# Optimization experiments

Hardware: AMD Instinct MI355X
Metric: run time of the kernel (lower is better)

## Reference

```python
import jax, jax.numpy as jnp
import numpy as np

B, P, N = 32, 64, 8192
EPS_CASE = 0.0001  # hard-coded threshold in fc_of_edge's tf.where


def setup_inputs() -> dict:
    key = jax.random.key(0)
    k1, k2 = jax.random.split(key)
    points = jax.random.normal(k1, (B, P, 2), dtype=jnp.float32)
    # phi grid comes from fc_tensor[0, 0, :] in the original ctor; use angles in [0, 2*pi)
    phi = jax.random.uniform(k2, (N,), dtype=jnp.float32) * (2.0 * np.pi)
    return {"points": points, "phi": phi}


def reference(points, phi):
    # q(phi) = [cos(phi), sin(phi) - 1], shape [2, N]
    q = jnp.stack([jnp.cos(phi), jnp.sin(phi) - 1.0])
    cross = jnp.array([[0.0, -1.0], [1.0, 0.0]], dtype=points.dtype)
    q_cross = cross @ q                                   # [2, N]
    scale = 1.0 / jnp.abs(q[0] ** 2 + q[1] ** 2)          # [N], real

    # vectorize the python edge loop: edge k is (points[:, k-1], points[:, k])
    p1 = points                                           # [B, P, 2]
    p0 = jnp.roll(points, 1, axis=1)                      # [B, P, 2]
    d = p1 - p0

    dot = lambda a, b: jnp.einsum('bpi,in->bpn', a, b)    # [B, P, N]
    dp0q = dot(p0, q)
    dp1q = dot(p1, q)
    ddq = dot(d, q)
    ddqc = dot(d, q_cross)

    j = jnp.complex64(1j)
    f_p0 = -jnp.exp(j * dp0q)                             # c = 0 in fc_of_phi
    f_p1 = -jnp.exp(j * dp1q)

    mask = jnp.abs(ddq) >= EPS_CASE
    ddq_safe = jnp.where(mask, ddq, 1.0)                  # avoid div-by-~0 in unused branch
    case1 = scale * ddqc * (f_p1 - f_p0) / ddq_safe
    case2 = scale * ddqc * (-j) * jnp.exp(j * dp0q)
    res = jnp.where(mask, case1, case2)                   # [B, P, N] complex64

    sum_res = jnp.sum(res, axis=1)                        # [B, N]
    # original: concat(real, imag) along axis=1 of [B, 1, N] -> [B, 2, N]
    return jnp.stack([jnp.real(sum_res), jnp.imag(sum_res)], axis=1)
```

## Files before the change

### kernel.cpp

```cpp
#include <hip/hip_runtime.h>
#include <math.h>

#define BATCH 32
#define PTS   64
#define NPHI  8192

__device__ __forceinline__ void fast_sincosf(double x, float* s, float* c) {
    const double TWO_OVER_PI = 6.36619772367581382433e-01;
    const double PIO2_HI     = 1.57079632679489661923e+00;
    const double PIO2_LO     = 6.12323399573676603587e-17;
    const double kd = __builtin_rint(x * TWO_OVER_PI);
    const int    qi = (int)kd;
    double r = __builtin_fma(-kd, PIO2_HI, x);
    r = __builtin_fma(-kd, PIO2_LO, r);
    const double r2 = r * r;

    double ps = 1.58969099521155010221e-10;
    ps = __builtin_fma(ps, r2, -2.50507602534068634195e-08);
    ps = __builtin_fma(ps, r2,  2.75573137070700676789e-06);
    ps = __builtin_fma(ps, r2, -1.98412698298579493134e-04);
    ps = __builtin_fma(ps, r2,  8.33333333332248946124e-03);
    ps = __builtin_fma(ps, r2, -1.66666666666666324348e-01);
    const double sinr = __builtin_fma(r * r2, ps, r);

    double pc = -1.13596475577881948265e-11;
    pc = __builtin_fma(pc, r2,  2.08757232129817482790e-09);
    pc = __builtin_fma(pc, r2, -2.75573143513906633035e-07);
    pc = __builtin_fma(pc, r2,  2.48015872894767294178e-05);
    pc = __builtin_fma(pc, r2, -1.38888888888741095749e-03);
    pc = __builtin_fma(pc, r2,  4.16666666666666019037e-02);
    const double cosr = __builtin_fma(r2 * r2, pc, __builtin_fma(-0.5, r2, 1.0));

    float sf = (float)sinr, cf = (float)cosr;
    const bool sw = (qi & 1);
    float ss = sw ? cf : sf;
    float cc = sw ? sf : cf;
    *s = (qi & 2)       ? -ss : ss;
    *c = ((qi + 1) & 2) ? -cc : cc;
}

__global__ __launch_bounds__(256) void scatter_polygon_kernel(
    const float* __restrict__ points,
    const float* __restrict__ phi,
    float* __restrict__ out)
{
    __shared__ float spts[2 * PTS];

    const int b = blockIdx.y;
    const int n = blockIdx.x * blockDim.x + threadIdx.x;

    if (threadIdx.x < 2 * PTS) {
        spts[threadIdx.x] = points[b * 2 * PTS + threadIdx.x];
    }
    __syncthreads();

    const float ph = phi[n];
    float sph, cph;
    fast_sincosf((double)ph, &sph, &cph);
    const float q0  = cph;
    const float q1  = __fsub_rn(sph, 1.0f);
    const float nq1 = -q1;
    const float scale =
        1.0f / fabsf(__fadd_rn(__fmul_rn(q0, q0), __fmul_rn(q1, q1)));

    float xp = spts[2 * (PTS - 1)];
    float yp = spts[2 * (PTS - 1) + 1];
    const float dp_prev = __fadd_rn(__fmul_rn(xp, q0), __fmul_rn(yp, q1));
    float s0, c0;
    fast_sincosf((double)dp_prev, &s0, &c0);

    double accR = 0.0, accI = 0.0;

    #pragma unroll 4
    for (int p = 0; p < PTS; ++p) {
        const float x = spts[2 * p];
        const float y = spts[2 * p + 1];
        const float dp_cur = __fadd_rn(__fmul_rn(x, q0), __fmul_rn(y, q1));
        float s1, c1;
        fast_sincosf((double)dp_cur, &s1, &c1);

        const float dx = __fsub_rn(x, xp);
        const float dy = __fsub_rn(y, yp);
        const float ddq  = __fadd_rn(__fmul_rn(dx, q0),  __fmul_rn(dy, q1));
        const float ddqc = __fadd_rn(__fmul_rn(dx, nq1), __fmul_rn(dy, q0));
        const float t = __fmul_rn(scale, ddqc);

        const float dR = __fsub_rn(c0, c1);
        const float dI = __fsub_rn(s0, s1);
        const bool  m1 = (fabsf(ddq) >= 1e-4f);
        const float ddq_safe = m1 ? ddq : 1.0f;
        const float r1R = __fdiv_rn(__fmul_rn(t, dR), ddq_safe);
        const float r1I = __fdiv_rn(__fmul_rn(t, dI), ddq_safe);
        const float r2R = __fmul_rn(t, s0);
        const float r2I = -__fmul_rn(t, c0);

        accR += (double)(m1 ? r1R : r2R);
        accI += (double)(m1 ? r1I : r2I);

        xp = x; yp = y; c0 = c1; s0 = s1;
    }

    out[(size_t)b * 2 * NPHI + n]        = (float)accR;
    out[(size_t)b * 2 * NPHI + NPHI + n] = (float)accI;
}

extern "C" void kernel_launch(void* const* d_in, const int* in_sizes, int n_in,
                              void* d_out, int out_size, void* d_ws, size_t ws_size,
                              hipStream_t stream) {
    const float* points = (const float*)d_in[0];
    const float* phi    = (const float*)d_in[1];
    float* out          = (float*)d_out;

    dim3 grid(NPHI / 256, BATCH);
    scatter_polygon_kernel<<<grid, 256, 0, stream>>>(points, phi, out);
}
```

Measured before the change: 88.30 us.

## Split polygon edge loop across thread pairs and cut double-precision work

Each phi value is now handled by two threads, each covering half of the polygon edges, and the partial sums are combined with a shuffle. Accumulation moves from double to float, the two IEEE divisions become one hardware reciprocal plus multiplies, and range reduction computes its quotient in float. The grid doubles in size and the launch bounds ask for higher occupancy. Each thread still evaluates the sincos of the polygon vertex just before its half, so that computation is duplicated. Float accumulation and the approximate reciprocal lower accuracy.

```diff
diff --git a/kernel.cpp b/kernel.cpp
--- a/kernel.cpp
+++ b/kernel.cpp
@@ -5,12 +5,15 @@
 #define PTS   64
 #define NPHI  8192
 
-__device__ __forceinline__ void fast_sincosf(double x, float* s, float* c) {
-    const double TWO_OVER_PI = 6.36619772367581382433e-01;
-    const double PIO2_HI     = 1.57079632679489661923e+00;
-    const double PIO2_LO     = 6.12323399573676603587e-17;
-    const double kd = __builtin_rint(x * TWO_OVER_PI);
-    const int    qi = (int)kd;
+__device__ __forceinline__ void fast_sincosf(float xf, float* s, float* c) {
+    const double PIO2_HI = 1.57079632679489661923e+00;
+    const double PIO2_LO = 6.12323399573676603587e-17;
+
+    const float kf = __builtin_rintf(__fmul_rn(xf, 0.63661977236758138243f));
+    const int   qi = (int)kf;
+    const double kd = (double)qi;
+    const double x  = (double)xf;
+
     double r = __builtin_fma(-kd, PIO2_HI, x);
     r = __builtin_fma(-kd, PIO2_LO, r);
     const double r2 = r * r;
@@ -31,15 +34,15 @@
     pc = __builtin_fma(pc, r2,  4.16666666666666019037e-02);
     const double cosr = __builtin_fma(r2 * r2, pc, __builtin_fma(-0.5, r2, 1.0));
 
-    float sf = (float)sinr, cf = (float)cosr;
+    const float sf = (float)sinr, cf = (float)cosr;
     const bool sw = (qi & 1);
-    float ss = sw ? cf : sf;
-    float cc = sw ? sf : cf;
+    const float ss = sw ? cf : sf;
+    const float cc = sw ? sf : cf;
     *s = (qi & 2)       ? -ss : ss;
     *c = ((qi + 1) & 2) ? -cc : cc;
 }
 
-__global__ __launch_bounds__(256) void scatter_polygon_kernel(
+__global__ __launch_bounds__(256, 8) void scatter_polygon_kernel(
     const float* __restrict__ points,
     const float* __restrict__ phi,
     float* __restrict__ out)
@@ -47,37 +50,42 @@
     __shared__ float spts[2 * PTS];
 
     const int b = blockIdx.y;
-    const int n = blockIdx.x * blockDim.x + threadIdx.x;
+    const int tid = threadIdx.x;
+    const int h = tid & 1;
+    const int n = blockIdx.x * 128 + (tid >> 1);
 
-    if (threadIdx.x < 2 * PTS) {
-        spts[threadIdx.x] = points[b * 2 * PTS + threadIdx.x];
+    if (tid < 2 * PTS) {
+        spts[tid] = points[b * 2 * PTS + tid];
     }
     __syncthreads();
 
     const float ph = phi[n];
     float sph, cph;
-    fast_sincosf((double)ph, &sph, &cph);
+    fast_sincosf(ph, &sph, &cph);
     const float q0  = cph;
     const float q1  = __fsub_rn(sph, 1.0f);
     const float nq1 = -q1;
     const float scale =
         1.0f / fabsf(__fadd_rn(__fmul_rn(q0, q0), __fmul_rn(q1, q1)));
 
-    float xp = spts[2 * (PTS - 1)];
-    float yp = spts[2 * (PTS - 1) + 1];
+    const int p0i = h ? (PTS / 2 - 1) : (PTS - 1);
+    float xp = spts[2 * p0i];
+    float yp = spts[2 * p0i + 1];
     const float dp_prev = __fadd_rn(__fmul_rn(xp, q0), __fmul_rn(yp, q1));
     float s0, c0;
-    fast_sincosf((double)dp_prev, &s0, &c0);
+    fast_sincosf(dp_prev, &s0, &c0);
 
-    double accR = 0.0, accI = 0.0;
+    float accR = 0.0f, accI = 0.0f;
+    const int pbase = h * (PTS / 2);
 
     #pragma unroll 4
-    for (int p = 0; p < PTS; ++p) {
+    for (int i = 0; i < PTS / 2; ++i) {
+        const int p = pbase + i;
         const float x = spts[2 * p];
         const float y = spts[2 * p + 1];
         const float dp_cur = __fadd_rn(__fmul_rn(x, q0), __fmul_rn(y, q1));
         float s1, c1;
-        fast_sincosf((double)dp_cur, &s1, &c1);
+        fast_sincosf(dp_cur, &s1, &c1);
 
         const float dx = __fsub_rn(x, xp);
         const float dy = __fsub_rn(y, yp);
@@ -88,20 +96,26 @@
         const float dR = __fsub_rn(c0, c1);
         const float dI = __fsub_rn(s0, s1);
         const bool  m1 = (fabsf(ddq) >= 1e-4f);
-        const float ddq_safe = m1 ? ddq : 1.0f;
-        const float r1R = __fdiv_rn(__fmul_rn(t, dR), ddq_safe);
-        const float r1I = __fdiv_rn(__fmul_rn(t, dI), ddq_safe);
-        const float r2R = __fmul_rn(t, s0);
-        const float r2I = -__fmul_rn(t, c0);
+        const float inv = __builtin_amdgcn_rcpf(m1 ? ddq : 1.0f);
+        const float ti = t * inv;
+        const float r1R = ti * dR;
+        const float r1I = ti * dI;
+        const float r2R = t * s0;
+        const float r2I = -t * c0;
 
-        accR += (double)(m1 ? r1R : r2R);
-        accI += (double)(m1 ? r1I : r2I);
+        accR += m1 ? r1R : r2R;
+        accI += m1 ? r1I : r2I;
 
         xp = x; yp = y; c0 = c1; s0 = s1;
     }
 
-    out[(size_t)b * 2 * NPHI + n]        = (float)accR;
-    out[(size_t)b * 2 * NPHI + NPHI + n] = (float)accI;
+    const float totR = accR + __shfl_xor(accR, 1);
+    const float totI = accI + __shfl_xor(accI, 1);
+
+    if (h == 0) {
+        out[(size_t)b * 2 * NPHI + n]        = totR;
+        out[(size_t)b * 2 * NPHI + NPHI + n] = totI;
+    }
 }
 
 extern "C" void kernel_launch(void* const* d_in, const int* in_sizes, int n_in,
@@ -111,6 +125,6 @@
     const float* phi    = (const float*)d_in[1];
     float* out          = (float*)d_out;
 
-    dim3 grid(NPHI / 256, BATCH);
+    dim3 grid(NPHI / 128, BATCH);
     scatter_polygon_kernel<<<grid, 256, 0, stream>>>(points, phi, out);
 }
```

New measurement: 80.16 us. -9.2%, faster.
